# Kernel tuning notes

Measured on AMD Instinct MI355X. Metric: run time of the kernel, lower is better.

## Reference

```python
import jax, jax.numpy as jnp
import numpy as np

M = 5  # init kwarg of InterestCandidateAttention


def setup_inputs() -> dict:
    key = jax.random.key(0)
    k1, k2, k3 = jax.random.split(key, 3)
    bs, K, d = 4096, 50, 256
    interest = jax.random.normal(k1, (bs, K, d), dtype=jnp.float32)
    candidate = jax.random.normal(k2, (bs, d), dtype=jnp.float32)
    counts = jax.random.randint(k3, (bs,), 1, 20, dtype=jnp.int64)
    return {
        "interest_representations": interest,
        "candidate_news_representation": candidate,
        "unique_category_counts": counts,
    }


def reference(interest_representations, candidate_news_representation, unique_category_counts):
    bs, K, d = interest_representations.shape
    # per-row dot-product scores: [bs, K]
    attn = jnp.einsum("bkd,bd->bk", interest_representations, candidate_news_representation)
    # dynamic K per sample: ceil(log2(M * count)) clamped to [1, K]
    counts = jnp.maximum(unique_category_counts, 1).astype(jnp.float32)
    dyn_K = jnp.clip(jnp.ceil(jnp.log2(M * counts)).astype(jnp.int32), 1, K)  # [bs]
    # rank-based top-k mask (vectorized replacement of per-sample topk loop)
    order = jnp.argsort(-attn, axis=-1)          # indices sorted by descending score
    ranks = jnp.argsort(order, axis=-1)          # rank of each element (0 = largest)
    mask = (ranks < dyn_K[:, None]).astype(attn.dtype)  # [bs, K]
    masked = attn * mask
    # masked weighted sum over interests -> [bs, d]
    user = jnp.einsum("bk,bkd->bd", masked, interest_representations)
    return user
```

## Files before the change

### kernel.cpp

```cpp
#include <hip/hip_runtime.h>

#define NK 50
#define D  256
#define NW 8
#define RPW 7

__global__ __launch_bounds__(512) void ica_kernel(
    const float* __restrict__ interest,
    const float* __restrict__ cand,
    const int*   __restrict__ counts,
    float*       __restrict__ out,
    int bs)
{
    const int b    = blockIdx.x;
    const int tid  = threadIdx.x;
    const int lane = tid & 63;
    const int wave = tid >> 6;

    __shared__ float s_attn[NK];
    __shared__ float s_w[NK];
    __shared__ float s_part[NW][D];

    const float* irow = interest + (size_t)b * NK * D;

    const float4 c4 = *reinterpret_cast<const float4*>(cand + (size_t)b * D + lane * 4);

    float4 frag[RPW];
    #pragma unroll
    for (int i = 0; i < RPW; ++i) {
        const int k = wave + i * NW;
        if (k < NK)
            frag[i] = *reinterpret_cast<const float4*>(irow + (size_t)k * D + lane * 4);
    }

    #pragma unroll
    for (int i = 0; i < RPW; ++i) {
        const int k = wave + i * NW;
        if (k < NK) {
            const float4 a4 = frag[i];
            float p = a4.x * c4.x + a4.y * c4.y + a4.z * c4.z + a4.w * c4.w;
            #pragma unroll
            for (int off = 32; off >= 1; off >>= 1)
                p += __shfl_xor(p, off, 64);
            if (lane == 0) s_attn[k] = p;
        }
    }
    __syncthreads();

    if (wave == 0) {
        int cnt = counts[b];
        if (cnt < 1) cnt = 1;
        int dynK = (int)ceilf(log2f(5.0f * (float)cnt));
        if (dynK < 1)  dynK = 1;
        if (dynK > NK) dynK = NK;

        if (lane < NK) {
            const float my = s_attn[lane];
            int rank = 0;
            #pragma unroll 1
            for (int j = 0; j < NK; ++j) {
                const float vj = s_attn[j];
                rank += (vj > my) || (vj == my && j < lane);
            }
            s_w[lane] = (rank < dynK) ? my : 0.0f;
        }
    }
    __syncthreads();

    float4 acc = {0.f, 0.f, 0.f, 0.f};
    #pragma unroll
    for (int i = 0; i < RPW; ++i) {
        const int k = wave + i * NW;
        if (k < NK) {
            const float w = s_w[k];
            acc.x += w * frag[i].x;
            acc.y += w * frag[i].y;
            acc.z += w * frag[i].z;
            acc.w += w * frag[i].w;
        }
    }
    *reinterpret_cast<float4*>(&s_part[wave][lane * 4]) = acc;
    __syncthreads();

    if (tid < D) {
        float r = 0.f;
        #pragma unroll
        for (int w = 0; w < NW; ++w)
            r += s_part[w][tid];
        out[(size_t)b * D + tid] = r;
    }
}

extern "C" void kernel_launch(void* const* d_in, const int* in_sizes, int n_in,
                              void* d_out, int out_size, void* d_ws, size_t ws_size,
                              hipStream_t stream) {
    const float* interest = (const float*)d_in[0];
    const float* cand     = (const float*)d_in[1];
    const int*   counts   = (const int*)d_in[2];
    float*       out      = (float*)d_out;

    const int bs = in_sizes[2];
    ica_kernel<<<bs, 512, 0, stream>>>(interest, cand, counts, out, bs);
}
```

Baseline: 38.28 us.

## Process two samples per block, prefetching second sample into LDS via global_load_lds

Each block now handles two batch rows. While the first row's scores, top-k mask and weighted sum are computed from registers, the second row's interest rows are loaded straight into LDS with global_load_lds, and a few late rows go into registers. The grid is halved. The goal is to hide memory latency behind compute, but the kernel now needs about 43KB of LDS per block, which may lower occupancy, and it relies on hand-written s_waitcnt/s_barrier sequences.

```diff
diff --git a/kernel.cpp b/kernel.cpp
--- a/kernel.cpp
+++ b/kernel.cpp
@@ -4,6 +4,17 @@
 #define D  256
 #define NW 8
 #define RPW 7
+#define LDSROWS 42
+
+typedef const __attribute__((address_space(1))) void* as1cv;
+typedef __attribute__((address_space(3))) void*       as3v;
+
+__device__ __forceinline__ void glds16(const float* g, float* s) {
+    __builtin_amdgcn_global_load_lds((as1cv)g, (as3v)s, 16, 0, 0);
+}
+
+#define BAR_LGKM() asm volatile("s_waitcnt lgkmcnt(0)\n\ts_barrier" ::: "memory")
+#define BAR_ALL()  asm volatile("s_waitcnt vmcnt(0) lgkmcnt(0)\n\ts_barrier" ::: "memory")
 
 __global__ __launch_bounds__(512) void ica_kernel(
     const float* __restrict__ interest,
@@ -12,48 +23,59 @@
     float*       __restrict__ out,
     int bs)
 {
-    const int b    = blockIdx.x;
     const int tid  = threadIdx.x;
     const int lane = tid & 63;
     const int wave = tid >> 6;
 
+    int sA = blockIdx.x * 2;
+    int sB = sA + 1;
+    if (sA >= bs) sA = bs - 1;
+    if (sB >= bs) sB = bs - 1;
+
     __shared__ float s_attn[NK];
     __shared__ float s_w[NK];
     __shared__ float s_part[NW][D];
+    __shared__ float s_bufB[LDSROWS * D];
 
-    const float* irow = interest + (size_t)b * NK * D;
+    const float* irowA = interest + (size_t)sA * NK * D;
+    const float* irowB = interest + (size_t)sB * NK * D;
 
-    const float4 c4 = *reinterpret_cast<const float4*>(cand + (size_t)b * D + lane * 4);
-
-    float4 frag[RPW];
+    const float4 c4A = *reinterpret_cast<const float4*>(cand + (size_t)sA * D + lane * 4);
+    float4 fragA[RPW];
     #pragma unroll
     for (int i = 0; i < RPW; ++i) {
         const int k = wave + i * NW;
         if (k < NK)
-            frag[i] = *reinterpret_cast<const float4*>(irow + (size_t)k * D + lane * 4);
+            fragA[i] = *reinterpret_cast<const float4*>(irowA + (size_t)k * D + lane * 4);
     }
+
+    #pragma unroll
+    for (int i = 0; i < 6; ++i) {
+        const int r = wave + i * NW;
+        if (r < LDSROWS)
+            glds16(irowB + (size_t)r * D + lane * 4, &s_bufB[r * D]);
+    }
+    const float4 c4B = *reinterpret_cast<const float4*>(cand + (size_t)sB * D + lane * 4);
+    const int cntA = counts[sA];
+    const int cntB = counts[sB];
 
     #pragma unroll
     for (int i = 0; i < RPW; ++i) {
         const int k = wave + i * NW;
         if (k < NK) {
-            const float4 a4 = frag[i];
-            float p = a4.x * c4.x + a4.y * c4.y + a4.z * c4.z + a4.w * c4.w;
+            const float4 a4 = fragA[i];
+            float p = a4.x*c4A.x + a4.y*c4A.y + a4.z*c4A.z + a4.w*c4A.w;
             #pragma unroll
-            for (int off = 32; off >= 1; off >>= 1)
-                p += __shfl_xor(p, off, 64);
+            for (int off = 32; off >= 1; off >>= 1) p += __shfl_xor(p, off, 64);
             if (lane == 0) s_attn[k] = p;
         }
     }
-    __syncthreads();
+    BAR_LGKM();
 
     if (wave == 0) {
-        int cnt = counts[b];
-        if (cnt < 1) cnt = 1;
+        int cnt = cntA < 1 ? 1 : cntA;
         int dynK = (int)ceilf(log2f(5.0f * (float)cnt));
-        if (dynK < 1)  dynK = 1;
-        if (dynK > NK) dynK = NK;
-
+        dynK = dynK < 1 ? 1 : (dynK > NK ? NK : dynK);
         if (lane < NK) {
             const float my = s_attn[lane];
             int rank = 0;
@@ -65,29 +87,95 @@
             s_w[lane] = (rank < dynK) ? my : 0.0f;
         }
     }
-    __syncthreads();
+    BAR_LGKM();
 
-    float4 acc = {0.f, 0.f, 0.f, 0.f};
+    {
+        float4 acc = {0.f, 0.f, 0.f, 0.f};
+        #pragma unroll
+        for (int i = 0; i < RPW; ++i) {
+            const int k = wave + i * NW;
+            if (k < NK) {
+                const float w = s_w[k];
+                acc.x += w * fragA[i].x;  acc.y += w * fragA[i].y;
+                acc.z += w * fragA[i].z;  acc.w += w * fragA[i].w;
+            }
+        }
+        *reinterpret_cast<float4*>(&s_part[wave][lane * 4]) = acc;
+    }
+    const int   lateK = (wave < 2) ? (48 + wave) : (40 + wave);
+    const float4 lateB = *reinterpret_cast<const float4*>(irowB + (size_t)lateK * D + lane * 4);
+    BAR_LGKM();
+
+    if (tid < D) {
+        float r = 0.f;
+        #pragma unroll
+        for (int w = 0; w < NW; ++w) r += s_part[w][tid];
+        out[(size_t)sA * D + tid] = r;
+    }
+
+    BAR_ALL();
+
+    float4 fragB[RPW];
     #pragma unroll
     for (int i = 0; i < RPW; ++i) {
         const int k = wave + i * NW;
         if (k < NK) {
-            const float w = s_w[k];
-            acc.x += w * frag[i].x;
-            acc.y += w * frag[i].y;
-            acc.z += w * frag[i].z;
-            acc.w += w * frag[i].w;
+            if (k < LDSROWS)
+                fragB[i] = *reinterpret_cast<const float4*>(&s_bufB[k * D + lane * 4]);
+            else
+                fragB[i] = lateB;
         }
     }
-    *reinterpret_cast<float4*>(&s_part[wave][lane * 4]) = acc;
-    __syncthreads();
+    #pragma unroll
+    for (int i = 0; i < RPW; ++i) {
+        const int k = wave + i * NW;
+        if (k < NK) {
+            const float4 a4 = fragB[i];
+            float p = a4.x*c4B.x + a4.y*c4B.y + a4.z*c4B.z + a4.w*c4B.w;
+            #pragma unroll
+            for (int off = 32; off >= 1; off >>= 1) p += __shfl_xor(p, off, 64);
+            if (lane == 0) s_attn[k] = p;
+        }
+    }
+    BAR_LGKM();
+
+    if (wave == 0) {
+        int cnt = cntB < 1 ? 1 : cntB;
+        int dynK = (int)ceilf(log2f(5.0f * (float)cnt));
+        dynK = dynK < 1 ? 1 : (dynK > NK ? NK : dynK);
+        if (lane < NK) {
+            const float my = s_attn[lane];
+            int rank = 0;
+            #pragma unroll 1
+            for (int j = 0; j < NK; ++j) {
+                const float vj = s_attn[j];
+                rank += (vj > my) || (vj == my && j < lane);
+            }
+            s_w[lane] = (rank < dynK) ? my : 0.0f;
+        }
+    }
+    BAR_LGKM();
+
+    {
+        float4 acc = {0.f, 0.f, 0.f, 0.f};
+        #pragma unroll
+        for (int i = 0; i < RPW; ++i) {
+            const int k = wave + i * NW;
+            if (k < NK) {
+                const float w = s_w[k];
+                acc.x += w * fragB[i].x;  acc.y += w * fragB[i].y;
+                acc.z += w * fragB[i].z;  acc.w += w * fragB[i].w;
+            }
+        }
+        *reinterpret_cast<float4*>(&s_part[wave][lane * 4]) = acc;
+    }
+    BAR_LGKM();
 
     if (tid < D) {
         float r = 0.f;
         #pragma unroll
-        for (int w = 0; w < NW; ++w)
-            r += s_part[w][tid];
-        out[(size_t)b * D + tid] = r;
+        for (int w = 0; w < NW; ++w) r += s_part[w][tid];
+        out[(size_t)sB * D + tid] = r;
     }
 }
 
@@ -99,6 +187,7 @@
     const int*   counts   = (const int*)d_in[2];
     float*       out      = (float*)d_out;
 
-    const int bs = in_sizes[2];
-    ica_kernel<<<bs, 512, 0, stream>>>(interest, cand, counts, out, bs);
+    const int bs   = in_sizes[2];
+    const int grid = (bs + 1) / 2;
+    ica_kernel<<<grid, 512, 0, stream>>>(interest, cand, counts, out, bs);
 }
```

New measurement: 47.54 us. 24.2% more time.
